# Performance work log

Hardware: AMD Instinct MI355X
Metric: run time of the kernel (lower is better)

Reference implementation:

```python
import jax, jax.numpy as jnp
import numpy as np

B, D, H, W = 32, 256, 32, 32
K = 1024

def setup_inputs() -> dict:
    key = jax.random.key(0)
    k1, k2 = jax.random.split(key)
    x = jax.random.normal(k1, (B, D, H, W), dtype=jnp.float32)
    codebook = jax.random.normal(k2, (K, D), dtype=jnp.float32)
    return {"x": x, "codebook": codebook}

def reference(x, codebook):
    b, lat, h, w = x.shape
    # (B, D, H, W) -> (B*H*W, D) tokens
    xt = jnp.transpose(x, (0, 2, 3, 1)).reshape(-1, lat)  # [N, D]
    # Squared euclidean distances via expansion (argmin-equivalent to cdist)
    x_sq = jnp.sum(xt * xt, axis=-1, keepdims=True)           # [N, 1]
    c_sq = jnp.sum(codebook * codebook, axis=-1)[None, :]     # [1, K]
    dist2 = x_sq - 2.0 * (xt @ codebook.T) + c_sq             # [N, K]
    idx = jnp.argmin(dist2, axis=-1)                          # [N]
    quant = codebook[idx]                                     # [N, D]
    codebook_loss = jnp.mean((jax.lax.stop_gradient(xt) - quant) ** 2)
    commitment_loss = jnp.mean((xt - jax.lax.stop_gradient(quant)) ** 2)
    # Straight-through estimator
    out = xt + jax.lax.stop_gradient(quant - xt)              # [N, D]
    out = out.reshape(b, h, w, lat).transpose(0, 3, 1, 2)     # [B, D, H, W]
    min_enc_idx = idx.reshape(b, h, w)                        # [B, H, W]
    return out, min_enc_idx, codebook_loss, commitment_loss
```

## Files before the change

kernel.cpp:

```cpp
#include <hip/hip_runtime.h>

#define B_   32
#define D_   256
#define HW_  1024
#define N_   32768
#define K_   1024
#define DHW  (D_ * HW_)
#define MARGIN 0.3f

typedef __attribute__((ext_vector_type(8)))  short bf16x8;
typedef __attribute__((ext_vector_type(16))) float f32x16;

union FragU { uint4 q; bf16x8 v; };

__device__ inline uint bf16rne(float x) {
    uint ub = __float_as_uint(x);
    return (ub + 0x7fffu + ((ub >> 16) & 1u)) >> 16;
}

__global__ __launch_bounds__(256)
void prep_cb(const float* __restrict__ cb, uint4* __restrict__ cbt2,
             float* __restrict__ csq, float* __restrict__ cbT,
             int* __restrict__ rcount, float* __restrict__ oloss) {
    __shared__ uint sh[256], sl[256];
    __shared__ float rr[4];
    const int k = blockIdx.x, d = threadIdx.x;
    float v = cb[(size_t)k * D_ + d];
    uint hb = bf16rne(v);
    float hf = __uint_as_float(hb << 16);
    uint lb = bf16rne(v - hf);
    sh[d] = hb; sl[d] = lb;
    cbT[(size_t)d * K_ + k] = v;
    float s = v * v;
    #pragma unroll
    for (int off = 32; off >= 1; off >>= 1) s += __shfl_xor(s, off, 64);
    if ((d & 63) == 0) rr[d >> 6] = s;
    __syncthreads();
    if (d == 0) csq[k] = (rr[0] + rr[1]) + (rr[2] + rr[3]);
    if (k == 0 && d == 0) { *rcount = 0; oloss[0] = 0.f; oloss[1] = 0.f; }
    if (d < 64) {
        const int ch = d >> 2, it = d & 3;
        const int p = it >> 1, h = it & 1;
        const int d0 = ch * 16 + h * 8;
        const uint* src = p ? sl : sh;
        uint w[4];
        #pragma unroll
        for (int jj = 0; jj < 4; ++jj)
            w[jj] = src[d0 + 2 * jj] | (src[d0 + 2 * jj + 1] << 16);
        cbt2[((ch * 4 + it) << 10) + k] = make_uint4(w[0], w[1], w[2], w[3]);
    }
}

#define DO_STEP(SA, SB, SC, SD, S) do {                                          \
    const int cc_ = cq * 4 + (S);                                                \
    const int ch_ = cc_ & 15;                                                    \
    FragU tf[4];                                                                 \
    _Pragma("unroll")                                                            \
    for (int j = 0; j < 4; ++j) tf[j].q = TkS[ch_ * 2 + sub][j * 32 + l31];      \
    __builtin_amdgcn_s_setprio(1);                                               \
    _Pragma("unroll")                                                            \
    for (int j = 0; j < 4; ++j)                                                  \
        acc[0][j] = __builtin_amdgcn_mfma_f32_32x32x16_bf16(SA.v, tf[j].v, acc[0][j], 0, 0, 0); \
    _Pragma("unroll")                                                            \
    for (int j = 0; j < 4; ++j)                                                  \
        acc[1][j] = __builtin_amdgcn_mfma_f32_32x32x16_bf16(SB.v, tf[j].v, acc[1][j], 0, 0, 0); \
    _Pragma("unroll")                                                            \
    for (int j = 0; j < 4; ++j)                                                  \
        acc[0][j] = __builtin_amdgcn_mfma_f32_32x32x16_bf16(SC.v, tf[j].v, acc[0][j], 0, 0, 0); \
    _Pragma("unroll")                                                            \
    for (int j = 0; j < 4; ++j)                                                  \
        acc[1][j] = __builtin_amdgcn_mfma_f32_32x32x16_bf16(SD.v, tf[j].v, acc[1][j], 0, 0, 0); \
    __builtin_amdgcn_s_setprio(0);                                               \
    if (cq < 7) {                                                                \
        const int nc_ = cc_ + 4;                                                 \
        const int noff_ = (((nc_ & 15) * 4) << 10) + ((nc_ >> 4) * 64);          \
        SA.q = cb_hi[noff_];      SB.q = cb_hi[noff_ + 32];                      \
        SC.q = cb_lo[noff_];      SD.q = cb_lo[noff_ + 32];                      \
    }                                                                            \
} while (0)

__global__ __launch_bounds__(512, 1)
void vq_main(const float* __restrict__ x, const uint4* __restrict__ cbt2,
             const float* __restrict__ csqg, const float* __restrict__ cb,
             int* __restrict__ rcount, int* __restrict__ rlist,
             float* __restrict__ bdist, float* __restrict__ out,
             float* __restrict__ oidx, float* __restrict__ oloss) {
    __shared__ __align__(16) uint SMEM[17408];
    uint4 (*TkS)[128] = reinterpret_cast<uint4(*)[128]>(SMEM);
    float* csqS = reinterpret_cast<float*>(SMEM + 16384);

    const int tid = threadIdx.x;
    const int lane = tid & 63;
    const int sub = lane >> 5, l31 = lane & 31;
    const int w = tid >> 6;
    const int tok0 = blockIdx.x * 128;
    const int bb = tok0 >> 10, hw0 = tok0 & 1023;

    csqS[tid] = csqg[tid];
    csqS[tid + 512] = csqg[tid + 512];

    const uint4* cb_hi = cbt2 + (sub << 10) + w * 128 + l31;
    const uint4* cb_lo = cbt2 + ((2 + sub) << 10) + w * 128 + l31;

    FragU p0a, p0b, p0c, p0d, p1a, p1b, p1c, p1d,
          p2a, p2b, p2c, p2d, p3a, p3b, p3c, p3d;
    p0a.q = cb_hi[0];         p0b.q = cb_hi[32];
    p0c.q = cb_lo[0];         p0d.q = cb_lo[32];
    p1a.q = cb_hi[1 << 12];   p1b.q = cb_hi[(1 << 12) + 32];
    p1c.q = cb_lo[1 << 12];   p1d.q = cb_lo[(1 << 12) + 32];
    p2a.q = cb_hi[2 << 12];   p2b.q = cb_hi[(2 << 12) + 32];
    p2c.q = cb_lo[2 << 12];   p2d.q = cb_lo[(2 << 12) + 32];
    p3a.q = cb_hi[3 << 12];   p3b.q = cb_hi[(3 << 12) + 32];
    p3c.q = cb_lo[3 << 12];   p3d.q = cb_lo[(3 << 12) + 32];

    {
        const int t = tid & 127;
        const int dgrp = tid >> 7;
        const float* xp = x + (size_t)bb * DHW + hw0 + t;
        #pragma unroll
        for (int i = 0; i < 8; ++i) {
            int g = i * 4 + dgrp;
            float v[8];
            #pragma unroll
            for (int e = 0; e < 8; ++e)
                v[e] = xp[(size_t)(g * 8 + e) * HW_];
            uint wd[4];
            #pragma unroll
            for (int jj = 0; jj < 4; ++jj)
                wd[jj] = bf16rne(v[2 * jj]) | (bf16rne(v[2 * jj + 1]) << 16);
            TkS[g][t] = make_uint4(wd[0], wd[1], wd[2], wd[3]);
        }
    }
    __syncthreads();

    f32x16 acc[2][4] = {};
    float v1[4], v2[4]; int k1[4];
    #pragma unroll
    for (int j = 0; j < 4; ++j) { v1[j] = 3.4e38f; v2[j] = 3.4e38f; k1[j] = 0; }

    for (int cq = 0; cq < 8; ++cq) {
        DO_STEP(p0a, p0b, p0c, p0d, 0);
        DO_STEP(p1a, p1b, p1c, p1d, 1);
        DO_STEP(p2a, p2b, p2c, p2d, 2);
        DO_STEP(p3a, p3b, p3c, p3d, 3);

        if ((cq & 3) == 3) {
            const int ct = cq >> 2;
            const int cbase = w * 128 + ct * 64 + sub * 4;
            #pragma unroll
            for (int f = 0; f < 2; ++f) {
                #pragma unroll
                for (int g8 = 0; g8 < 4; ++g8) {
                    float4 cs4 = *reinterpret_cast<const float4*>(&csqS[cbase + f * 32 + g8 * 8]);
                    const float csa[4] = {cs4.x, cs4.y, cs4.z, cs4.w};
                    #pragma unroll
                    for (int q = 0; q < 4; ++q) {
                        int code = cbase + f * 32 + g8 * 8 + q;
                        int r = g8 * 4 + q;
                        #pragma unroll
                        for (int j = 0; j < 4; ++j) {
                            float s = fmaf(-2.f, acc[f][j][r], csa[q]);
                            bool c = s < v1[j];
                            v2[j] = c ? v1[j] : fminf(v2[j], s);
                            k1[j] = c ? code : k1[j];
                            v1[j] = c ? s : v1[j];
                        }
                    }
                }
            }
            const f32x16 zf = {};
            #pragma unroll
            for (int f = 0; f < 2; ++f)
                #pragma unroll
                for (int j = 0; j < 4; ++j) acc[f][j] = zf;
        }
    }

    #pragma unroll
    for (int j = 0; j < 4; ++j) {
        float ov1 = __shfl_xor(v1[j], 32, 64);
        float ov2 = __shfl_xor(v2[j], 32, 64);
        int   ok1 = __shfl_xor(k1[j], 32, 64);
        float nv2 = fminf(fminf(v2[j], ov2), fmaxf(v1[j], ov1));
        if (ov1 < v1[j] || (ov1 == v1[j] && ok1 < k1[j])) { v1[j] = ov1; k1[j] = ok1; }
        v2[j] = nv2;
    }
    __syncthreads();
    float* red = reinterpret_cast<float*>(SMEM);
    int* bestk_s = reinterpret_cast<int*>(SMEM + 17280);
    if (sub == 0) {
        #pragma unroll
        for (int j = 0; j < 4; ++j) {
            int t = j * 32 + l31;
            red[(w * 128 + t) * 3 + 0] = v1[j];
            red[(w * 128 + t) * 3 + 1] = v2[j];
            red[(w * 128 + t) * 3 + 2] = __int_as_float(k1[j]);
        }
    }
    __syncthreads();
    if (tid < 128) {
        float bv1 = red[tid * 3], bv2 = red[tid * 3 + 1];
        int bk = __float_as_int(red[tid * 3 + 2]);
        #pragma unroll
        for (int m = 1; m < 8; ++m) {
            float a1 = red[(m * 128 + tid) * 3], a2 = red[(m * 128 + tid) * 3 + 1];
            int ak = __float_as_int(red[(m * 128 + tid) * 3 + 2]);
            float nv2 = fminf(fminf(bv2, a2), fmaxf(bv1, a1));
            if (a1 < bv1 || (a1 == bv1 && ak < bk)) { bv1 = a1; bk = ak; }
            bv2 = nv2;
        }
        int n = tok0 + tid;
        bestk_s[tid] = bk;
        bdist[n] = bv1;
        oidx[n] = (float)bk;
        if (bv2 - bv1 < MARGIN) rlist[atomicAdd(rcount, 1)] = n;
        float v = bv1;
        #pragma unroll
        for (int off = 32; off >= 1; off >>= 1) v += __shfl_xor(v, off, 64);
        if ((tid & 63) == 0) {
            float t2 = v * (1.0f / 8388608.0f);
            atomicAdd(&oloss[0], t2);
            atomicAdd(&oloss[1], t2);
        }
    }
    __syncthreads();

    float* S2 = reinterpret_cast<float*>(SMEM);
    #pragma unroll 1
    for (int h = 0; h < 2; ++h) {
        #pragma unroll
        for (int i = 0; i < 8; ++i) {
            int r = w * 8 + i;
            int kk = bestk_s[h * 64 + r];
            float4 cw4 = *reinterpret_cast<const float4*>(cb + (size_t)kk * D_ + lane * 4);
            *reinterpret_cast<float4*>(&S2[r * 260 + lane * 4]) = cw4;
        }
        __syncthreads();
        {
            const int q = tid & 15, dg = tid >> 4;
            const size_t obase = (size_t)bb * DHW + hw0 + h * 64 + q * 4;
            #pragma unroll
            for (int dd = 0; dd < 8; ++dd) {
                int d = dg * 8 + dd;
                float4 wv;
                wv.x = S2[(q * 4 + 0) * 260 + d];
                wv.y = S2[(q * 4 + 1) * 260 + d];
                wv.z = S2[(q * 4 + 2) * 260 + d];
                wv.w = S2[(q * 4 + 3) * 260 + d];
                *reinterpret_cast<float4*>(out + obase + (size_t)d * HW_) = wv;
            }
        }
        __syncthreads();
    }
}

__global__ __launch_bounds__(256)
void vq_refine(const float* __restrict__ x, const float* __restrict__ cb,
               const float* __restrict__ cbT, const float* __restrict__ csq,
               const int* __restrict__ rcount, const int* __restrict__ rlist,
               const float* __restrict__ bdist, float* __restrict__ out,
               float* __restrict__ oidx, float* __restrict__ oloss) {
    __shared__ float xv[8][256];
    __shared__ float xsq[8];
    __shared__ float wredv[4][8];
    __shared__ int   wredk[4][8];
    __shared__ int   kfin[8];
    const int tid = threadIdx.x;
    const int cnt = min(rcount[0], N_);
    for (int base = blockIdx.x * 8; base < cnt; base += gridDim.x * 8) {
        const int m = min(8, cnt - base);
        __syncthreads();
        for (int j = 0; j < m; ++j) {
            int n = rlist[base + j];
            int b = n >> 10, hw = n & 1023;
            xv[j][tid] = x[(size_t)b * DHW + (size_t)tid * HW_ + hw];
        }
        for (int j = m; j < 8; ++j) xv[j][tid] = 0.f;
        __syncthreads();
        {
            int g = tid >> 5, l = tid & 31;
            float s = 0.f;
            #pragma unroll
            for (int d8 = 0; d8 < 8; ++d8) { float v = xv[g][d8 * 32 + l]; s = fmaf(v, v, s); }
            #pragma unroll
            for (int mm = 1; mm < 32; mm <<= 1) s += __shfl_xor(s, mm, 64);
            if (l == 0) xsq[g] = s;
        }
        __syncthreads();

        float dots[4][8];
        #pragma unroll
        for (int c4 = 0; c4 < 4; ++c4)
            #pragma unroll
            for (int j = 0; j < 8; ++j) dots[c4][j] = 0.f;

        const float* cbase = cbT + tid;
        for (int d0 = 0; d0 < 256; d0 += 8) {
            float xr[8][8];
            #pragma unroll
            for (int j = 0; j < 8; ++j) {
                float4 a = *reinterpret_cast<const float4*>(&xv[j][d0]);
                float4 b = *reinterpret_cast<const float4*>(&xv[j][d0 + 4]);
                xr[j][0] = a.x; xr[j][1] = a.y; xr[j][2] = a.z; xr[j][3] = a.w;
                xr[j][4] = b.x; xr[j][5] = b.y; xr[j][6] = b.z; xr[j][7] = b.w;
            }
            #pragma unroll
            for (int c4 = 0; c4 < 4; ++c4) {
                float cv[8];
                #pragma unroll
                for (int u = 0; u < 8; ++u)
                    cv[u] = cbase[(size_t)(d0 + u) * K_ + c4 * 256];
                #pragma unroll
                for (int u = 0; u < 8; ++u)
                    #pragma unroll
                    for (int j = 0; j < 8; ++j)
                        dots[c4][j] = fmaf(cv[u], xr[j][u], dots[c4][j]);
            }
        }

        float bv[8]; int bk[8];
        #pragma unroll
        for (int j = 0; j < 8; ++j) { bv[j] = 3.4e38f; bk[j] = 0; }
        #pragma unroll
        for (int c4 = 0; c4 < 4; ++c4) {
            const int code = c4 * 256 + tid;
            const float cs = csq[code];
            #pragma unroll
            for (int j = 0; j < 8; ++j) {
                float dist = fmaf(-2.f, dots[c4][j], xsq[j]) + cs;
                if (dist < bv[j]) { bv[j] = dist; bk[j] = code; }
            }
        }
        #pragma unroll
        for (int j = 0; j < 8; ++j) {
            if (j < m) {
                float v = bv[j]; int k = bk[j];
                #pragma unroll
                for (int mm = 1; mm < 64; mm <<= 1) {
                    float ov = __shfl_xor(v, mm, 64);
                    int   ok = __shfl_xor(k, mm, 64);
                    if (ov < v || (ov == v && ok < k)) { v = ov; k = ok; }
                }
                if ((tid & 63) == 0) { wredv[tid >> 6][j] = v; wredk[tid >> 6][j] = k; }
            }
        }
        __syncthreads();
        if (tid < m) {
            float v = wredv[0][tid]; int k = wredk[0][tid];
            #pragma unroll
            for (int q = 1; q < 4; ++q) {
                if (wredv[q][tid] < v || (wredv[q][tid] == v && wredk[q][tid] < k)) {
                    v = wredv[q][tid]; k = wredk[q][tid];
                }
            }
            int n = rlist[base + tid];
            kfin[tid] = k;
            oidx[n] = (float)k;
            float delta = (v - bdist[n]) * (1.0f / 8388608.0f);
            atomicAdd(&oloss[0], delta);
            atomicAdd(&oloss[1], delta);
        }
        __syncthreads();
        for (int j = 0; j < m; ++j) {
            int n = rlist[base + j];
            int b = n >> 10, hw = n & 1023;
            out[(size_t)b * DHW + (size_t)tid * HW_ + hw] = cb[(size_t)kfin[j] * D_ + tid];
        }
        __syncthreads();
    }
}

extern "C" void kernel_launch(void* const* d_in, const int* in_sizes, int n_in,
                              void* d_out, int out_size, void* d_ws, size_t ws_size,
                              hipStream_t stream) {
    const float* x  = (const float*)d_in[0];
    const float* cb = (const float*)d_in[1];

    float* out   = (float*)d_out;
    float* oidx  = out + 8388608;
    float* oloss = out + 8388608 + 32768;

    uint* wsb = (uint*)d_ws;
    uint4*  cbt2  = (uint4*)wsb;
    float*  csq   = (float*)(wsb + 262144);
    float*  cbT   = (float*)(wsb + 263168);
    int*    rcount= (int*)  (wsb + 525312);
    int*    rlist = (int*)  (wsb + 525316);
    float*  bdist = (float*)(wsb + 558084);

    prep_cb <<<1024, 256, 0, stream>>>(cb, cbt2, csq, cbT, rcount, oloss);
    vq_main <<<256, 512, 0, stream>>>(x, cbt2, csq, cb, rcount, rlist, bdist, out, oidx, oloss);
    vq_refine<<<256, 256, 0, stream>>>(x, cb, cbT, csq, rcount, rlist, bdist, out, oidx, oloss);
}
```

Baseline: 106.7 us.

## Split vq_main work across 16 waves per block with smaller per-wave tiles

vq_main now runs 1024 threads per block. Each wave handles 64 codes by 64 tokens instead of 128 by 128, so accumulator state is halved. The explicit register prefetch pipeline for codebook fragments is removed; fragments are now loaded inside the unrolled step loop. The refine kernel grid is doubled. The aim is more waves per CU to hide latency, at the cost of losing software prefetch and adding register pressure from the tighter launch bounds.

New measurement: 133.8 us. +25.4%, slower.

```diff
diff --git a/kernel.cpp b/kernel.cpp
--- a/kernel.cpp
+++ b/kernel.cpp
@@ -12,6 +12,8 @@
 typedef __attribute__((ext_vector_type(16))) float f32x16;
 
 union FragU { uint4 q; bf16x8 v; };
+
+#define MFMA32 __builtin_amdgcn_mfma_f32_32x32x16_bf16
 
 __device__ inline uint bf16rne(float x) {
     uint ub = __float_as_uint(x);
@@ -51,35 +53,7 @@
     }
 }
 
-#define DO_STEP(SA, SB, SC, SD, S) do {                                          \
-    const int cc_ = cq * 4 + (S);                                                \
-    const int ch_ = cc_ & 15;                                                    \
-    FragU tf[4];                                                                 \
-    _Pragma("unroll")                                                            \
-    for (int j = 0; j < 4; ++j) tf[j].q = TkS[ch_ * 2 + sub][j * 32 + l31];      \
-    __builtin_amdgcn_s_setprio(1);                                               \
-    _Pragma("unroll")                                                            \
-    for (int j = 0; j < 4; ++j)                                                  \
-        acc[0][j] = __builtin_amdgcn_mfma_f32_32x32x16_bf16(SA.v, tf[j].v, acc[0][j], 0, 0, 0); \
-    _Pragma("unroll")                                                            \
-    for (int j = 0; j < 4; ++j)                                                  \
-        acc[1][j] = __builtin_amdgcn_mfma_f32_32x32x16_bf16(SB.v, tf[j].v, acc[1][j], 0, 0, 0); \
-    _Pragma("unroll")                                                            \
-    for (int j = 0; j < 4; ++j)                                                  \
-        acc[0][j] = __builtin_amdgcn_mfma_f32_32x32x16_bf16(SC.v, tf[j].v, acc[0][j], 0, 0, 0); \
-    _Pragma("unroll")                                                            \
-    for (int j = 0; j < 4; ++j)                                                  \
-        acc[1][j] = __builtin_amdgcn_mfma_f32_32x32x16_bf16(SD.v, tf[j].v, acc[1][j], 0, 0, 0); \
-    __builtin_amdgcn_s_setprio(0);                                               \
-    if (cq < 7) {                                                                \
-        const int nc_ = cc_ + 4;                                                 \
-        const int noff_ = (((nc_ & 15) * 4) << 10) + ((nc_ >> 4) * 64);          \
-        SA.q = cb_hi[noff_];      SB.q = cb_hi[noff_ + 32];                      \
-        SC.q = cb_lo[noff_];      SD.q = cb_lo[noff_ + 32];                      \
-    }                                                                            \
-} while (0)
-
-__global__ __launch_bounds__(512, 1)
+__global__ __launch_bounds__(1024, 4)
 void vq_main(const float* __restrict__ x, const uint4* __restrict__ cbt2,
              const float* __restrict__ csqg, const float* __restrict__ cb,
              int* __restrict__ rcount, int* __restrict__ rlist,
@@ -93,33 +67,20 @@
     const int lane = tid & 63;
     const int sub = lane >> 5, l31 = lane & 31;
     const int w = tid >> 6;
+    const int th = w & 1;
+    const int cs = w >> 1;
     const int tok0 = blockIdx.x * 128;
     const int bb = tok0 >> 10, hw0 = tok0 & 1023;
 
     csqS[tid] = csqg[tid];
-    csqS[tid + 512] = csqg[tid + 512];
-
-    const uint4* cb_hi = cbt2 + (sub << 10) + w * 128 + l31;
-    const uint4* cb_lo = cbt2 + ((2 + sub) << 10) + w * 128 + l31;
-
-    FragU p0a, p0b, p0c, p0d, p1a, p1b, p1c, p1d,
-          p2a, p2b, p2c, p2d, p3a, p3b, p3c, p3d;
-    p0a.q = cb_hi[0];         p0b.q = cb_hi[32];
-    p0c.q = cb_lo[0];         p0d.q = cb_lo[32];
-    p1a.q = cb_hi[1 << 12];   p1b.q = cb_hi[(1 << 12) + 32];
-    p1c.q = cb_lo[1 << 12];   p1d.q = cb_lo[(1 << 12) + 32];
-    p2a.q = cb_hi[2 << 12];   p2b.q = cb_hi[(2 << 12) + 32];
-    p2c.q = cb_lo[2 << 12];   p2d.q = cb_lo[(2 << 12) + 32];
-    p3a.q = cb_hi[3 << 12];   p3b.q = cb_hi[(3 << 12) + 32];
-    p3c.q = cb_lo[3 << 12];   p3d.q = cb_lo[(3 << 12) + 32];
 
     {
         const int t = tid & 127;
         const int dgrp = tid >> 7;
         const float* xp = x + (size_t)bb * DHW + hw0 + t;
         #pragma unroll
-        for (int i = 0; i < 8; ++i) {
-            int g = i * 4 + dgrp;
+        for (int i = 0; i < 4; ++i) {
+            int g = i * 8 + dgrp;
             float v[8];
             #pragma unroll
             for (int e = 0; e < 8; ++e)
@@ -133,37 +94,53 @@
     }
     __syncthreads();
 
-    f32x16 acc[2][4] = {};
-    float v1[4], v2[4]; int k1[4];
+    f32x16 acc[2][2] = {};
+    float v1[2] = {3.4e38f, 3.4e38f}, v2[2] = {3.4e38f, 3.4e38f};
+    int k1[2] = {0, 0};
+
+    const uint4* cbh = cbt2 + (sub << 10) + cs * 64 + l31;
+    const uint4* cbl = cbt2 + ((2 + sub) << 10) + cs * 64 + l31;
+
     #pragma unroll
-    for (int j = 0; j < 4; ++j) { v1[j] = 3.4e38f; v2[j] = 3.4e38f; k1[j] = 0; }
-
-    for (int cq = 0; cq < 8; ++cq) {
-        DO_STEP(p0a, p0b, p0c, p0d, 0);
-        DO_STEP(p1a, p1b, p1c, p1d, 1);
-        DO_STEP(p2a, p2b, p2c, p2d, 2);
-        DO_STEP(p3a, p3b, p3c, p3d, 3);
-
-        if ((cq & 3) == 3) {
-            const int ct = cq >> 2;
-            const int cbase = w * 128 + ct * 64 + sub * 4;
+    for (int s = 0; s < 32; ++s) {
+        const int p = s >> 4, ch = s & 15;
+        const int off = ((ch * 4) << 10) + p * 512;
+        FragU ah0, ah1, al0, al1, tf0, tf1;
+        ah0.q = cbh[off];        ah1.q = cbh[off + 32];
+        al0.q = cbl[off];        al1.q = cbl[off + 32];
+        tf0.q = TkS[ch * 2 + sub][th * 64 + l31];
+        tf1.q = TkS[ch * 2 + sub][th * 64 + 32 + l31];
+
+        __builtin_amdgcn_s_setprio(1);
+        acc[0][0] = MFMA32(ah0.v, tf0.v, acc[0][0], 0, 0, 0);
+        acc[0][1] = MFMA32(ah0.v, tf1.v, acc[0][1], 0, 0, 0);
+        acc[1][0] = MFMA32(ah1.v, tf0.v, acc[1][0], 0, 0, 0);
+        acc[1][1] = MFMA32(ah1.v, tf1.v, acc[1][1], 0, 0, 0);
+        acc[0][0] = MFMA32(al0.v, tf0.v, acc[0][0], 0, 0, 0);
+        acc[0][1] = MFMA32(al0.v, tf1.v, acc[0][1], 0, 0, 0);
+        acc[1][0] = MFMA32(al1.v, tf0.v, acc[1][0], 0, 0, 0);
+        acc[1][1] = MFMA32(al1.v, tf1.v, acc[1][1], 0, 0, 0);
+        __builtin_amdgcn_s_setprio(0);
+
+        if (ch == 15) {
+            const int cgbase = p * 512 + cs * 64 + sub * 4;
             #pragma unroll
             for (int f = 0; f < 2; ++f) {
                 #pragma unroll
                 for (int g8 = 0; g8 < 4; ++g8) {
-                    float4 cs4 = *reinterpret_cast<const float4*>(&csqS[cbase + f * 32 + g8 * 8]);
+                    float4 cs4 = *reinterpret_cast<const float4*>(&csqS[cgbase + f * 32 + g8 * 8]);
                     const float csa[4] = {cs4.x, cs4.y, cs4.z, cs4.w};
                     #pragma unroll
                     for (int q = 0; q < 4; ++q) {
-                        int code = cbase + f * 32 + g8 * 8 + q;
+                        int code = cgbase + f * 32 + g8 * 8 + q;
                         int r = g8 * 4 + q;
                         #pragma unroll
-                        for (int j = 0; j < 4; ++j) {
-                            float s = fmaf(-2.f, acc[f][j][r], csa[q]);
-                            bool c = s < v1[j];
-                            v2[j] = c ? v1[j] : fminf(v2[j], s);
+                        for (int j = 0; j < 2; ++j) {
+                            float sd = fmaf(-2.f, acc[f][j][r], csa[q]);
+                            bool c = sd < v1[j];
+                            v2[j] = c ? v1[j] : fminf(v2[j], sd);
                             k1[j] = c ? code : k1[j];
-                            v1[j] = c ? s : v1[j];
+                            v1[j] = c ? sd : v1[j];
                         }
                     }
                 }
@@ -172,12 +149,12 @@
             #pragma unroll
             for (int f = 0; f < 2; ++f)
                 #pragma unroll
-                for (int j = 0; j < 4; ++j) acc[f][j] = zf;
+                for (int j = 0; j < 2; ++j) acc[f][j] = zf;
         }
     }
 
     #pragma unroll
-    for (int j = 0; j < 4; ++j) {
+    for (int j = 0; j < 2; ++j) {
         float ov1 = __shfl_xor(v1[j], 32, 64);
         float ov2 = __shfl_xor(v2[j], 32, 64);
         int   ok1 = __shfl_xor(k1[j], 32, 64);
@@ -190,11 +167,11 @@
     int* bestk_s = reinterpret_cast<int*>(SMEM + 17280);
     if (sub == 0) {
         #pragma unroll
-        for (int j = 0; j < 4; ++j) {
-            int t = j * 32 + l31;
-            red[(w * 128 + t) * 3 + 0] = v1[j];
-            red[(w * 128 + t) * 3 + 1] = v2[j];
-            red[(w * 128 + t) * 3 + 2] = __int_as_float(k1[j]);
+        for (int j = 0; j < 2; ++j) {
+            int t = th * 64 + j * 32 + l31;
+            red[(cs * 128 + t) * 3 + 0] = v1[j];
+            red[(cs * 128 + t) * 3 + 1] = v2[j];
+            red[(cs * 128 + t) * 3 + 2] = __int_as_float(k1[j]);
         }
     }
     __syncthreads();
@@ -229,8 +206,8 @@
     #pragma unroll 1
     for (int h = 0; h < 2; ++h) {
         #pragma unroll
-        for (int i = 0; i < 8; ++i) {
-            int r = w * 8 + i;
+        for (int i = 0; i < 4; ++i) {
+            int r = w * 4 + i;
             int kk = bestk_s[h * 64 + r];
             float4 cw4 = *reinterpret_cast<const float4*>(cb + (size_t)kk * D_ + lane * 4);
             *reinterpret_cast<float4*>(&S2[r * 260 + lane * 4]) = cw4;
@@ -240,8 +217,8 @@
             const int q = tid & 15, dg = tid >> 4;
             const size_t obase = (size_t)bb * DHW + hw0 + h * 64 + q * 4;
             #pragma unroll
-            for (int dd = 0; dd < 8; ++dd) {
-                int d = dg * 8 + dd;
+            for (int dd = 0; dd < 4; ++dd) {
+                int d = dg * 4 + dd;
                 float4 wv;
                 wv.x = S2[(q * 4 + 0) * 260 + d];
                 wv.y = S2[(q * 4 + 1) * 260 + d];
@@ -389,6 +366,6 @@
     float*  bdist = (float*)(wsb + 558084);
 
     prep_cb <<<1024, 256, 0, stream>>>(cb, cbt2, csq, cbT, rcount, oloss);
-    vq_main <<<256, 512, 0, stream>>>(x, cbt2, csq, cb, rcount, rlist, bdist, out, oidx, oloss);
-    vq_refine<<<256, 256, 0, stream>>>(x, cb, cbT, csq, rcount, rlist, bdist, out, oidx, oloss);
-}
+    vq_main <<<256, 1024, 0, stream>>>(x, cbt2, csq, cb, rcount, rlist, bdist, out, oidx, oloss);
+    vq_refine<<<512, 256, 0, stream>>>(x, cb, cbT, csq, rcount, rlist, bdist, out, oidx, oloss);
+}
```
